# Kernel tuning notes

Hardware: AMD Instinct MI355X
Metric: run time of the kernel (lower is better)

Reference implementation:

```python
import jax, jax.numpy as jnp
import numpy as np

HEADS = 4
CH = 64  # hidden_channels (per-head out channels)
N_INT = 50000
N_LANE = 400000
E_PO = 400000
E_ADJ = 200000


def setup_inputs() -> dict:
    key = jax.random.key(0)
    ks = iter(jax.random.split(key, 32))
    rn = lambda shape, s=0.1: jax.random.normal(next(ks), shape, dtype=jnp.float32) * s
    inp = {
        'x_int': rn((N_INT, 16), 1.0),
        'x_lane': rn((N_LANE, 12), 1.0),
        'h0': jnp.zeros((N_INT, CH), jnp.float32),
        'enc_int_W': rn((16, CH)), 'enc_int_b': jnp.zeros((CH,), jnp.float32),
        'enc_lane_W': rn((12, CH)), 'enc_lane_b': jnp.zeros((CH,), jnp.float32),
        'Wsrc_po': rn((CH, HEADS * CH)), 'Wdst_po': rn((CH, HEADS * CH)),
        'att_src_po': rn((HEADS, CH)), 'att_dst_po': rn((HEADS, CH)),
        'bias_po': jnp.zeros((HEADS * CH,), jnp.float32),
        'Wsrc_adj': rn((CH, HEADS * CH)), 'Wdst_adj': rn((CH, HEADS * CH)),
        'att_src_adj': rn((HEADS, CH)), 'att_dst_adj': rn((HEADS, CH)),
        'bias_adj': jnp.zeros((HEADS * CH,), jnp.float32),
        'gru_W_ih': rn((3 * CH, HEADS * CH)), 'gru_W_hh': rn((3 * CH, CH)),
        'gru_b_ih': jnp.zeros((3 * CH,), jnp.float32), 'gru_b_hh': jnp.zeros((3 * CH,), jnp.float32),
        'W_pi': rn((CH, 8)), 'b_pi': jnp.zeros((8,), jnp.float32),
        'W_v': rn((CH, 1)), 'b_v': jnp.zeros((1,), jnp.float32),
        'src_po': jax.random.randint(next(ks), (E_PO,), 0, N_LANE),
        'dst_po': jax.random.randint(next(ks), (E_PO,), 0, N_INT),
        'src_adj': jax.random.randint(next(ks), (E_ADJ,), 0, N_INT),
        'dst_adj': jax.random.randint(next(ks), (E_ADJ,), 0, N_INT),
    }
    return inp


def gat_conv(x_src, x_dst, src, dst, Wsrc, Wdst, a_src, a_dst, bias, n_dst):
    # PyG GATConv (bipartite, concat=True, no self loops), negative_slope=0.2
    hs = (x_src @ Wsrc).reshape(-1, HEADS, CH)  # [Ns,H,C]
    hd = (x_dst @ Wdst).reshape(-1, HEADS, CH)  # [Nd,H,C]
    a_s = jnp.einsum('nhc,hc->nh', hs, a_src)   # [Ns,H]
    a_d = jnp.einsum('nhc,hc->nh', hd, a_dst)   # [Nd,H]
    alpha = jax.nn.leaky_relu(a_s[src] + a_d[dst], 0.2)        # [E,H]
    amax = jax.ops.segment_max(alpha, dst, num_segments=n_dst)  # [Nd,H]
    ex = jnp.exp(alpha - amax[dst])
    den = jax.ops.segment_sum(ex, dst, num_segments=n_dst)
    w = ex / den[dst]                                           # [E,H] softmax per dst
    msg = hs[src] * w[:, :, None]                               # [E,H,C]
    out = jax.ops.segment_sum(msg, dst, num_segments=n_dst)     # [Nd,H,C]
    return out.reshape(n_dst, HEADS * CH) + bias


def gru_cell(x, h, W_ih, W_hh, b_ih, b_hh):
    gi = x @ W_ih.T + b_ih
    gh = h @ W_hh.T + b_hh
    i_r, i_z, i_n = jnp.split(gi, 3, axis=1)
    h_r, h_z, h_n = jnp.split(gh, 3, axis=1)
    r = jax.nn.sigmoid(i_r + h_r)
    z = jax.nn.sigmoid(i_z + h_z)
    n = jnp.tanh(i_n + r * h_n)
    return (1.0 - z) * n + z * h


def reference(x_int, x_lane, h0, enc_int_W, enc_int_b, enc_lane_W, enc_lane_b,
              Wsrc_po, Wdst_po, att_src_po, att_dst_po, bias_po,
              Wsrc_adj, Wdst_adj, att_src_adj, att_dst_adj, bias_adj,
              gru_W_ih, gru_W_hh, gru_b_ih, gru_b_hh,
              W_pi, b_pi, W_v, b_v,
              src_po, dst_po, src_adj, dst_adj):
    # per-type encoders + ReLU
    e_int = jax.nn.relu(x_int @ enc_int_W + enc_int_b)    # [N_int,CH]
    e_lane = jax.nn.relu(x_lane @ enc_lane_W + enc_lane_b)  # [N_lane,CH]
    # HeteroConv aggr='sum' over relations targeting 'intersection'
    o_po = gat_conv(e_lane, e_int, src_po, dst_po, Wsrc_po, Wdst_po,
                    att_src_po, att_dst_po, bias_po, N_INT)
    o_adj = gat_conv(e_int, e_int, src_adj, dst_adj, Wsrc_adj, Wdst_adj,
                     att_src_adj, att_dst_adj, bias_adj, N_INT)
    inter = jax.nn.relu(o_po + o_adj)  # dropout = identity (deterministic eval)
    h_new = gru_cell(inter, h0, gru_W_ih, gru_W_hh, gru_b_ih, gru_b_hh)
    logits = h_new @ W_pi + b_pi
    value = h_new @ W_v + b_v
    return logits, value, h_new
```

## Files before the change

### kernel.cpp

```cpp
#include <hip/hip_runtime.h>

#define NI 50000
#define NL 400000
#define EPO 400000
#define EADJ 200000
#define NLB 1563
#define NIB 196

typedef unsigned int u32;
typedef unsigned short u16;
typedef short bf16x8 __attribute__((ext_vector_type(8)));
typedef float f32x4 __attribute__((ext_vector_type(4)));

__device__ __forceinline__ float bf2f(u16 h){ return __uint_as_float(((u32)h)<<16); }
__device__ __forceinline__ u16 f2bf(float f){
  u32 u = __float_as_uint(f);
  u += 0x7FFFu + ((u>>16)&1u);
  return (u16)(u>>16);
}
__device__ __forceinline__ u32 pack2(float a, float b){
  return (u32)f2bf(a) | ((u32)f2bf(b)<<16);
}

__device__ __forceinline__ float b2_val(
    const float* __restrict__ W_ih, const float* __restrict__ W_hh, int m, int k)
{
  if(k < 256){ return (m<192) ? W_ih[m*256+k] : 0.f; }
  int kk = k-256;
  if(m<128) return W_hh[m*64+kk];
  if(m>=192) return W_hh[(m-64)*64+kk];
  return 0.f;
}

__global__ __launch_bounds__(256) void k0_prep(
    const float* __restrict__ Wsrc_po, const float* __restrict__ att_src_po,
    const float* __restrict__ Wdst_po, const float* __restrict__ att_dst_po,
    const float* __restrict__ Wsrc_adj, const float* __restrict__ att_src_adj,
    const float* __restrict__ Wdst_adj, const float* __restrict__ att_dst_adj,
    const float* __restrict__ W_ih, const float* __restrict__ W_hh,
    const float* __restrict__ bias_po, const float* __restrict__ bias_adj,
    const float* __restrict__ b_ih, const float* __restrict__ b_hh,
    float* __restrict__ v4, u16* __restrict__ WheadT, u16* __restrict__ B2F,
    float* __restrict__ bias_comb, float* __restrict__ bias2,
    int* __restrict__ cnt)
{
  const int T0 = 1024, T1 = 4*64*128, T2 = 10*16*64*8;
  const int TC = 2*NI;
  int total = T0 + T1 + T2 + 256 + 256 + TC;
  for(int t = blockIdx.x*256 + threadIdx.x; t < total; t += gridDim.x*256){
    if(t < T0){
      int which = t>>8, hc = t&255, h = hc>>6, c = hc&63;
      const float *W, *att;
      if(which==0){ W=Wsrc_po;  att=att_src_po; }
      else if(which==1){ W=Wdst_po;  att=att_dst_po; }
      else if(which==2){ W=Wsrc_adj; att=att_src_adj; }
      else { W=Wdst_adj; att=att_dst_adj; }
      float s=0.f;
      for(int j=0;j<64;j++) s += W[c*256 + h*64 + j]*att[h*64+j];
      v4[which*256 + hc] = s;
    } else if(t < T0 + T1){
      int i = t - T0; int h = i>>13, rem = i&8191, m = rem>>7, k = rem&127;
      float val = (k<64) ? Wsrc_po[k*256 + h*64 + m]
                         : Wsrc_adj[(k-64)*256 + h*64 + m];
      WheadT[i] = f2bf(val);
    } else if(t < T0 + T1 + T2){
      int i = t - (T0+T1);
      int j = i&7;
      int u4 = i>>3;
      int kstep = u4>>10, rem = u4&1023, tile = rem>>6, lane = rem&63;
      int col = tile*16 + (lane&15);
      int k = kstep*32 + (lane>>4)*8 + j;
      B2F[i] = f2bf(b2_val(W_ih, W_hh, col, k));
    } else if(t < T0 + T1 + T2 + 256){
      int m = t - (T0+T1+T2);
      bias_comb[m] = bias_po[m] + bias_adj[m];
    } else if(t < T0 + T1 + T2 + 512){
      int m = t - (T0+T1+T2+256);
      float v;
      if(m<128) v = b_ih[m] + b_hh[m];
      else if(m<192) v = b_ih[m];
      else v = b_hh[m-64];
      bias2[m] = v;
    } else {
      cnt[t - (T0+T1+T2+512)] = 0;
    }
  }
}

__global__ __launch_bounds__(256) void k_enc(
    const float* __restrict__ x_lane, const float* __restrict__ Wl, const float* __restrict__ bl,
    const float* __restrict__ x_int,  const float* __restrict__ Wi, const float* __restrict__ bi,
    const float* __restrict__ v_sp, const float* __restrict__ v_dp,
    const float* __restrict__ v_sa, const float* __restrict__ v_da,
    u16* __restrict__ e_lane, float* __restrict__ a_s_po,
    u16* __restrict__ e_int, float* __restrict__ a_dp, float* __restrict__ a_sa,
    float* __restrict__ a_da)
{
  __shared__ uint4 st4[8][256];
  int t = threadIdx.x;
  int blk = blockIdx.x;
  if(blk < NLB){
    int row = blk*256 + t;
    float xv[12];
    if(row < NL){
      const float4* xp = (const float4*)(x_lane + (size_t)row*12);
      float4 x0 = xp[0], x1 = xp[1], x2 = xp[2];
      xv[0]=x0.x; xv[1]=x0.y; xv[2]=x0.z; xv[3]=x0.w;
      xv[4]=x1.x; xv[5]=x1.y; xv[6]=x1.z; xv[7]=x1.w;
      xv[8]=x2.x; xv[9]=x2.y; xv[10]=x2.z; xv[11]=x2.w;
    } else {
#pragma unroll
      for(int k=0;k<12;k++) xv[k]=0.f;
    }
    float as0=0.f, as1=0.f, as2=0.f, as3=0.f;
#pragma unroll
    for(int c8=0;c8<8;c8++){
      float acc[8];
#pragma unroll
      for(int j=0;j<8;j++) acc[j]=bl[c8*8+j];
#pragma unroll
      for(int k=0;k<12;k++){
        float xk = xv[k];
#pragma unroll
        for(int j=0;j<8;j++) acc[j] += xk*Wl[k*64 + c8*8 + j];
      }
      float e[8];
#pragma unroll
      for(int j=0;j<8;j++){
        e[j] = fmaxf(acc[j], 0.f);
        int c = c8*8+j;
        as0 += e[j]*v_sp[c];
        as1 += e[j]*v_sp[64+c];
        as2 += e[j]*v_sp[128+c];
        as3 += e[j]*v_sp[192+c];
      }
      uint4 P;
      P.x = pack2(e[0],e[1]); P.y = pack2(e[2],e[3]);
      P.z = pack2(e[4],e[5]); P.w = pack2(e[6],e[7]);
      st4[c8][t] = P;
    }
    if(row < NL){
      float4 A; A.x=as0; A.y=as1; A.z=as2; A.w=as3;
      *(float4*)(a_s_po + (size_t)row*4) = A;
    }
    __syncthreads();
    uint4* outp = (uint4*)e_lane + (size_t)blk*2048;
    int rowlim = NL - blk*256;
#pragma unroll
    for(int i=0;i<8;i++){
      int idx = i*256 + t;
      int r = idx>>3, g = idx&7;
      if(r < rowlim) outp[idx] = st4[g][r];
    }
  } else {
    int b2 = blk - NLB;
    int row = b2*256 + t;
    float xv[16];
    if(row < NI){
      const float4* xp = (const float4*)(x_int + (size_t)row*16);
#pragma unroll
      for(int q=0;q<4;q++){
        float4 xq = xp[q];
        xv[q*4]=xq.x; xv[q*4+1]=xq.y; xv[q*4+2]=xq.z; xv[q*4+3]=xq.w;
      }
    } else {
#pragma unroll
      for(int k=0;k<16;k++) xv[k]=0.f;
    }
    float ad0=0,ad1=0,ad2=0,ad3=0, sa0=0,sa1=0,sa2=0,sa3=0, da0=0,da1=0,da2=0,da3=0;
#pragma unroll
    for(int c8=0;c8<8;c8++){
      float acc[8];
#pragma unroll
      for(int j=0;j<8;j++) acc[j]=bi[c8*8+j];
#pragma unroll
      for(int k=0;k<16;k++){
        float xk = xv[k];
#pragma unroll
        for(int j=0;j<8;j++) acc[j] += xk*Wi[k*64 + c8*8 + j];
      }
      float e[8];
#pragma unroll
      for(int j=0;j<8;j++){
        e[j] = fmaxf(acc[j], 0.f);
        int c = c8*8+j;
        ad0 += e[j]*v_dp[c];   ad1 += e[j]*v_dp[64+c];  ad2 += e[j]*v_dp[128+c];  ad3 += e[j]*v_dp[192+c];
        sa0 += e[j]*v_sa[c];   sa1 += e[j]*v_sa[64+c];  sa2 += e[j]*v_sa[128+c];  sa3 += e[j]*v_sa[192+c];
        da0 += e[j]*v_da[c];   da1 += e[j]*v_da[64+c];  da2 += e[j]*v_da[128+c];  da3 += e[j]*v_da[192+c];
      }
      uint4 P;
      P.x = pack2(e[0],e[1]); P.y = pack2(e[2],e[3]);
      P.z = pack2(e[4],e[5]); P.w = pack2(e[6],e[7]);
      st4[c8][t] = P;
    }
    if(row < NI){
      float4 A;
      A.x=ad0; A.y=ad1; A.z=ad2; A.w=ad3; *(float4*)(a_dp + (size_t)row*4) = A;
      A.x=sa0; A.y=sa1; A.z=sa2; A.w=sa3; *(float4*)(a_sa + (size_t)row*4) = A;
      A.x=da0; A.y=da1; A.z=da2; A.w=da3; *(float4*)(a_da + (size_t)row*4) = A;
    }
    __syncthreads();
    uint4* outp = (uint4*)e_int + (size_t)b2*2048;
    int rowlim = NI - b2*256;
#pragma unroll
    for(int i=0;i<8;i++){
      int idx = i*256 + t;
      int r = idx>>3, g = idx&7;
      if(r < rowlim) outp[idx] = st4[g][r];
    }
  }
}

__global__ __launch_bounds__(256) void k3_hist(
    const int* __restrict__ dst_po, const int* __restrict__ dst_adj, int* __restrict__ cnt)
{
  int i = blockIdx.x*256 + threadIdx.x;
  if(i < EPO) atomicAdd(&cnt[dst_po[i]], 1);
  else if(i < EPO+EADJ) atomicAdd(&cnt[NI + dst_adj[i-EPO]], 1);
}

__global__ __launch_bounds__(1024) void k4a_scan(
    const int* __restrict__ cnt, int* __restrict__ offA, int* __restrict__ bsum)
{
  __shared__ int s[1024];
  int y = blockIdx.y;
  int i = blockIdx.x*1024 + threadIdx.x;
  int v = (i<NI) ? cnt[y*NI+i] : 0;
  s[threadIdx.x]=v;
  __syncthreads();
  for(int o=1;o<1024;o<<=1){
    int t = (threadIdx.x>=o) ? s[threadIdx.x-o] : 0;
    __syncthreads();
    s[threadIdx.x] += t;
    __syncthreads();
  }
  if(i<NI) offA[y*NI+i] = s[threadIdx.x]-v;
  if(threadIdx.x==1023) bsum[y*64+blockIdx.x] = s[1023];
}

__global__ __launch_bounds__(128) void k4b_scanb(int* __restrict__ bsum)
{
  int y = threadIdx.x>>6, lane = threadIdx.x&63;
  int v = (lane<49) ? bsum[y*64+lane] : 0;
  int orig = v;
#pragma unroll
  for(int o=1;o<64;o<<=1){
    int t = __shfl_up(v,o,64);
    if(lane>=o) v += t;
  }
  if(lane<49) bsum[y*64+lane] = v-orig;
}

__global__ __launch_bounds__(1024) void k4c_add(
    int* __restrict__ offA, int* __restrict__ cur, const int* __restrict__ bsum)
{
  int y = blockIdx.y;
  int i = blockIdx.x*1024 + threadIdx.x;
  if(i<NI){
    int o = offA[y*NI+i] + bsum[y*64+blockIdx.x];
    offA[y*NI+i]=o;
    cur[y*NI+i]=o;
  }
}

__global__ __launch_bounds__(256) void k5_scatter(
    const int* __restrict__ src_po, const int* __restrict__ dst_po,
    const int* __restrict__ src_adj, const int* __restrict__ dst_adj,
    const float* __restrict__ a_s_po, const float* __restrict__ a_d_po,
    const float* __restrict__ a_s_adj, const float* __restrict__ a_d_adj,
    int* __restrict__ cur, int* __restrict__ csr_po, int* __restrict__ csr_adj,
    float* __restrict__ pw_po, float* __restrict__ pw_adj)
{
  int i = blockIdx.x*256 + threadIdx.x;
  if(i < EPO){
    int s = src_po[i];
    int d = dst_po[i];
    int p = atomicAdd(&cur[d],1);
    csr_po[p] = s;
    float4 as = *(const float4*)(a_s_po + (size_t)s*4);
    float4 ad = *(const float4*)(a_d_po + (size_t)d*4);
    float4 pv;
    float x;
    x = as.x+ad.x; pv.x = __expf(x>0.f?x:0.2f*x);
    x = as.y+ad.y; pv.y = __expf(x>0.f?x:0.2f*x);
    x = as.z+ad.z; pv.z = __expf(x>0.f?x:0.2f*x);
    x = as.w+ad.w; pv.w = __expf(x>0.f?x:0.2f*x);
    *(float4*)(pw_po + (size_t)p*4) = pv;
  } else if(i < EPO+EADJ){
    int e = i-EPO;
    int s = src_adj[e];
    int d = dst_adj[e];
    int p = atomicAdd(&cur[NI+d],1);
    csr_adj[p] = s;
    float4 as = *(const float4*)(a_s_adj + (size_t)s*4);
    float4 ad = *(const float4*)(a_d_adj + (size_t)d*4);
    float4 pv;
    float x;
    x = as.x+ad.x; pv.x = __expf(x>0.f?x:0.2f*x);
    x = as.y+ad.y; pv.y = __expf(x>0.f?x:0.2f*x);
    x = as.z+ad.z; pv.z = __expf(x>0.f?x:0.2f*x);
    x = as.w+ad.w; pv.w = __expf(x>0.f?x:0.2f*x);
    *(float4*)(pw_adj + (size_t)p*4) = pv;
  }
}

__device__ __forceinline__ void agg_rel(
    int beg, int n, int lane,
    const int* __restrict__ csr, const float* __restrict__ pw,
    const u16* __restrict__ emat, u16* __restrict__ aggrow)
{
  float l0=0,l1=0,l2=0,l3=0;
  float c0=0,c1=0,c2=0,c3=0;
  for(int base=0;base<n;base+=64){
    int m = n-base; if(m>64) m=64;
    int sv_ = (lane<m) ? csr[beg+base+lane] : 0;
    int t2=0;
    for(; t2+1<m; t2+=2){
      int s0 = __shfl(sv_, t2, 64);
      int s1 = __shfl(sv_, t2+1, 64);
      float4 p0 = *(const float4*)(pw + (size_t)(beg+base+t2)*4);
      float4 p1 = *(const float4*)(pw + (size_t)(beg+base+t2+1)*4);
      float e0 = bf2f(emat[(size_t)s0*64+lane]);
      float e1 = bf2f(emat[(size_t)s1*64+lane]);
      c0 += p0.x*e0; c1 += p0.y*e0; c2 += p0.z*e0; c3 += p0.w*e0;
      l0 += p0.x;    l1 += p0.y;    l2 += p0.z;    l3 += p0.w;
      c0 += p1.x*e1; c1 += p1.y*e1; c2 += p1.z*e1; c3 += p1.w*e1;
      l0 += p1.x;    l1 += p1.y;    l2 += p1.z;    l3 += p1.w;
    }
    if(t2<m){
      int s0 = __shfl(sv_, t2, 64);
      float4 p0 = *(const float4*)(pw + (size_t)(beg+base+t2)*4);
      float e0 = bf2f(emat[(size_t)s0*64+lane]);
      c0 += p0.x*e0; c1 += p0.y*e0; c2 += p0.z*e0; c3 += p0.w*e0;
      l0 += p0.x;    l1 += p0.y;    l2 += p0.z;    l3 += p0.w;
    }
  }
  aggrow[lane]       = f2bf(n>0 ? c0/l0 : 0.f);
  aggrow[64+lane]    = f2bf(n>0 ? c1/l1 : 0.f);
  aggrow[128+lane]   = f2bf(n>0 ? c2/l2 : 0.f);
  aggrow[192+lane]   = f2bf(n>0 ? c3/l3 : 0.f);
}

__global__ __launch_bounds__(256) void k6_agg(
    const int* __restrict__ off, const int* __restrict__ cnt,
    const int* __restrict__ csr_po, const int* __restrict__ csr_adj,
    const float* __restrict__ pw_po, const float* __restrict__ pw_adj,
    const u16* __restrict__ e_lane, const u16* __restrict__ e_int,
    u16* __restrict__ agg)
{
  int wave=threadIdx.x>>6, lane=threadIdx.x&63;
  int d = blockIdx.x*4 + wave;
  if(d>=NI) return;
  agg_rel(off[d],    cnt[d],    lane, csr_po,  pw_po,  e_lane, agg + (size_t)d*512);
  agg_rel(off[NI+d], cnt[NI+d], lane, csr_adj, pw_adj, e_int,  agg + (size_t)d*512 + 256);
}

__global__ __launch_bounds__(256) void gemm_head(
    const u16* __restrict__ agg, const u16* __restrict__ WheadT,
    const float* __restrict__ bias, u16* __restrict__ inter256)
{
  __shared__ u16 As[64][136];
  __shared__ u16 Bs[64][136];
  int t=threadIdx.x, wave=t>>6, lane=t&63;
  int h = blockIdx.y;
  int row0 = blockIdx.x*64;
  int r = lane&15, q = lane>>4;
  const uint4* Bsrc = (const uint4*)(WheadT + (size_t)h*8192);
#pragma unroll
  for(int it=0; it<4; it++){
    int idx = it*256 + t;
    int brow = idx>>4, u4 = idx&15;
    *(uint4*)&Bs[brow][u4*8] = Bsrc[idx];
    int grow = row0 + brow;
    uint4 v = {0,0,0,0};
    if(grow < NI){
      int co = (u4<8) ? (h*64 + u4*8) : (256 + h*64 + (u4-8)*8);
      v = *(const uint4*)(agg + (size_t)grow*512 + co);
    }
    *(uint4*)&As[brow][u4*8] = v;
  }
  __syncthreads();
  f32x4 acc0={0,0,0,0}, acc1={0,0,0,0}, acc2={0,0,0,0}, acc3={0,0,0,0};
#pragma unroll
  for(int ks=0; ks<4; ks++){
    bf16x8 af = *(const bf16x8*)&As[wave*16 + r][q*8 + ks*32];
    bf16x8 b0 = *(const bf16x8*)&Bs[ 0 + r][q*8 + ks*32];
    bf16x8 b1 = *(const bf16x8*)&Bs[16 + r][q*8 + ks*32];
    bf16x8 b2 = *(const bf16x8*)&Bs[32 + r][q*8 + ks*32];
    bf16x8 b3 = *(const bf16x8*)&Bs[48 + r][q*8 + ks*32];
    acc0 = __builtin_amdgcn_mfma_f32_16x16x32_bf16(af,b0,acc0,0,0,0);
    acc1 = __builtin_amdgcn_mfma_f32_16x16x32_bf16(af,b1,acc1,0,0,0);
    acc2 = __builtin_amdgcn_mfma_f32_16x16x32_bf16(af,b2,acc2,0,0,0);
    acc3 = __builtin_amdgcn_mfma_f32_16x16x32_bf16(af,b3,acc3,0,0,0);
  }
  int crow_base = row0 + wave*16 + q*4;
#pragma unroll
  for(int t2=0;t2<4;t2++){
    f32x4 a = (t2==0)?acc0 : (t2==1)?acc1 : (t2==2)?acc2 : acc3;
    int col = h*64 + t2*16 + r;
    float bcol = bias[col];
#pragma unroll
    for(int rr=0;rr<4;rr++){
      int row = crow_base + rr;
      if(row < NI)
        inter256[(size_t)row*256 + col] = f2bf(fmaxf(a[rr]+bcol, 0.f));
    }
  }
}

__global__ __launch_bounds__(256) void k9_gru(
    const u16* __restrict__ inter256, const uint4* __restrict__ B2F,
    const float* __restrict__ bias2, const float* __restrict__ h0,
    const float* __restrict__ Wpi, const float* __restrict__ bpi,
    const float* __restrict__ Wv, const float* __restrict__ bvp,
    float* __restrict__ out)
{
  int t=threadIdx.x, w=t>>6, lane=t&63;
  int r = lane&15, q = lane>>4;
  int row0 = blockIdx.x*64;
  int arow = row0 + w*16 + r;
  int arc = arow < NI ? arow : NI-1;
  const u16* Aptr = inter256 + (size_t)arc*256 + q*8;
  const float* h0r = h0 + (size_t)arc*64 + q*8;
  f32x4 acc[16];
#pragma unroll
  for(int i=0;i<16;i++) acc[i] = (f32x4){0,0,0,0};
#pragma unroll
  for(int ks=0; ks<10; ks++){
    bf16x8 af;
    if(ks < 8){
      af = *(const bf16x8*)(Aptr + ks*32);
    } else {
      const float* hp = h0r + (ks-8)*32;
      float4 f0 = *(const float4*)(hp);
      float4 f1 = *(const float4*)(hp+4);
      uint4 P;
      P.x = pack2(f0.x,f0.y); P.y = pack2(f0.z,f0.w);
      P.z = pack2(f1.x,f1.y); P.w = pack2(f1.z,f1.w);
      *(uint4*)&af = P;
    }
    const uint4* bp = B2F + ks*1024 + lane;
#pragma unroll
    for(int tt=0;tt<16;tt++){
      uint4 bu = bp[tt*64];
      bf16x8 bf; *(uint4*)&bf = bu;
      acc[tt] = __builtin_amdgcn_mfma_f32_16x16x32_bf16(af, bf, acc[tt], 0,0,0);
    }
  }
  float pk[4][8];
  float pv[4];
#pragma unroll
  for(int rr=0;rr<4;rr++){
    pv[rr]=0.f;
#pragma unroll
    for(int j=0;j<8;j++) pk[rr][j]=0.f;
  }
  int rbase = row0 + w*16 + q*4;
#pragma unroll
  for(int t2=0;t2<4;t2++){
    int c = t2*16 + r;
    float b0 = bias2[c], b1 = bias2[64+c], b2 = bias2[128+c], b3 = bias2[192+c];
    float wp[8];
#pragma unroll
    for(int j=0;j<8;j++) wp[j] = Wpi[c*8+j];
    float wv = Wv[c];
#pragma unroll
    for(int rr=0;rr<4;rr++){
      int row = rbase + rr;
      float g0 = acc[t2][rr]    + b0;
      float g1 = acc[t2+4][rr]  + b1;
      float g2 = acc[t2+8][rr]  + b2;
      float g3 = acc[t2+12][rr] + b3;
      float h0v = (row < NI) ? h0[(size_t)row*64 + c] : 0.f;
      float rg = 1.f/(1.f+__expf(-g0));
      float zg = 1.f/(1.f+__expf(-g1));
      float e2 = __expf(2.f*(g2 + rg*g3));
      float ng = 1.f - 2.f/(e2+1.f);
      float h = (1.f-zg)*ng + zg*h0v;
      if(row < NI) out[450000 + (size_t)row*64 + c] = h;
#pragma unroll
      for(int j=0;j<8;j++) pk[rr][j] += h*wp[j];
      pv[rr] += h*wv;
    }
  }
#pragma unroll
  for(int o=1;o<16;o<<=1){
#pragma unroll
    for(int rr=0;rr<4;rr++){
#pragma unroll
      for(int j=0;j<8;j++) pk[rr][j] += __shfl_xor(pk[rr][j], o, 64);
      pv[rr] += __shfl_xor(pv[rr], o, 64);
    }
  }
  if(r==0){
#pragma unroll
    for(int rr=0;rr<4;rr++){
      int row = rbase + rr;
      if(row < NI){
#pragma unroll
        for(int j=0;j<8;j++) out[(size_t)row*8 + j] = pk[rr][j] + bpi[j];
        out[400000 + row] = pv[rr] + bvp[0];
      }
    }
  }
}

extern "C" void kernel_launch(void* const* d_in, const int* in_sizes, int n_in,
                              void* d_out, int out_size, void* d_ws, size_t ws_size,
                              hipStream_t stream) {
  const float* x_int      = (const float*)d_in[0];
  const float* x_lane     = (const float*)d_in[1];
  const float* h0         = (const float*)d_in[2];
  const float* enc_int_W  = (const float*)d_in[3];
  const float* enc_int_b  = (const float*)d_in[4];
  const float* enc_lane_W = (const float*)d_in[5];
  const float* enc_lane_b = (const float*)d_in[6];
  const float* Wsrc_po    = (const float*)d_in[7];
  const float* Wdst_po    = (const float*)d_in[8];
  const float* att_src_po = (const float*)d_in[9];
  const float* att_dst_po = (const float*)d_in[10];
  const float* bias_po    = (const float*)d_in[11];
  const float* Wsrc_adj   = (const float*)d_in[12];
  const float* Wdst_adj   = (const float*)d_in[13];
  const float* att_src_adj= (const float*)d_in[14];
  const float* att_dst_adj= (const float*)d_in[15];
  const float* bias_adj   = (const float*)d_in[16];
  const float* gru_W_ih   = (const float*)d_in[17];
  const float* gru_W_hh   = (const float*)d_in[18];
  const float* gru_b_ih   = (const float*)d_in[19];
  const float* gru_b_hh   = (const float*)d_in[20];
  const float* W_pi       = (const float*)d_in[21];
  const float* b_pi       = (const float*)d_in[22];
  const float* W_v        = (const float*)d_in[23];
  const float* b_v        = (const float*)d_in[24];
  const int* src_po  = (const int*)d_in[25];
  const int* dst_po  = (const int*)d_in[26];
  const int* src_adj = (const int*)d_in[27];
  const int* dst_adj = (const int*)d_in[28];
  float* out = (float*)d_out;

  char* w = (char*)d_ws;
  size_t ofs = 0;
  auto alloc = [&](size_t bytes)->char*{
    char* p = w + ofs;
    ofs = (ofs + bytes + 255) & ~(size_t)255;
    return p;
  };
  u16*  e_lane   = (u16*)alloc((size_t)NL*64*2);
  u16*  e_int    = (u16*)alloc((size_t)NI*64*2);
  float* a_s_po  = (float*)alloc((size_t)NL*4*4);
  float* a_d_po  = (float*)alloc((size_t)NI*4*4);
  float* a_s_adj = (float*)alloc((size_t)NI*4*4);
  float* a_d_adj = (float*)alloc((size_t)NI*4*4);
  int*  cnt      = (int*)alloc((size_t)2*NI*4);
  int*  offA     = (int*)alloc((size_t)2*NI*4);
  int*  cur      = (int*)alloc((size_t)2*NI*4);
  int*  csr_po   = (int*)alloc((size_t)EPO*4);
  int*  csr_adj  = (int*)alloc((size_t)EADJ*4);
  float* pw_po   = (float*)alloc((size_t)EPO*4*4);
  float* pw_adj  = (float*)alloc((size_t)EADJ*4*4);
  int*  bsum     = (int*)alloc(2*64*4);
  u16*  agg      = (u16*)alloc((size_t)NI*512*2);
  u16*  inter256 = (u16*)alloc((size_t)NI*256*2);
  u16*  WheadT   = (u16*)alloc(4*64*128*2);
  u16*  B2F      = (u16*)alloc(10*16*64*8*2);
  float* v4      = (float*)alloc(4*256*4);
  float* bias_comb = (float*)alloc(256*4);
  float* bias2   = (float*)alloc(256*4);
  (void)ws_size; (void)n_in; (void)in_sizes; (void)out_size;

  k0_prep<<<256, 256, 0, stream>>>(
      Wsrc_po, att_src_po, Wdst_po, att_dst_po,
      Wsrc_adj, att_src_adj, Wdst_adj, att_dst_adj,
      gru_W_ih, gru_W_hh, bias_po, bias_adj, gru_b_ih, gru_b_hh,
      v4, WheadT, B2F, bias_comb, bias2, cnt);
  k_enc<<<NLB+NIB, 256, 0, stream>>>(
      x_lane, enc_lane_W, enc_lane_b,
      x_int, enc_int_W, enc_int_b,
      v4 + 0, v4 + 256, v4 + 512, v4 + 768,
      e_lane, a_s_po, e_int, a_d_po, a_s_adj, a_d_adj);
  k3_hist<<<(EPO+EADJ+255)/256, 256, 0, stream>>>(dst_po, dst_adj, cnt);
  k4a_scan<<<dim3(49,2), 1024, 0, stream>>>(cnt, offA, bsum);
  k4b_scanb<<<1, 128, 0, stream>>>(bsum);
  k4c_add<<<dim3(49,2), 1024, 0, stream>>>(offA, cur, bsum);
  k5_scatter<<<(EPO+EADJ+255)/256, 256, 0, stream>>>(src_po, dst_po, src_adj, dst_adj,
      a_s_po, a_d_po, a_s_adj, a_d_adj,
      cur, csr_po, csr_adj, pw_po, pw_adj);
  k6_agg<<<(NI+3)/4, 256, 0, stream>>>(offA, cnt, csr_po, csr_adj,
      pw_po, pw_adj, e_lane, e_int, agg);
  gemm_head<<<dim3((NI+63)/64, 4), 256, 0, stream>>>(agg, WheadT, bias_comb, inter256);
  k9_gru<<<(NI+63)/64, 256, 0, stream>>>(inter256, (const uint4*)B2F, bias2, h0,
      W_pi, b_pi, W_v, b_v, out);
}
```

Baseline: 379.9 us.

## Split encoder into lane/int kernels with 8 threads per row and shuffle reductions

Replaces the fused encoder kernel (one thread per row computing all 64 channels, then staging through LDS) with two kernels. In each, 8 threads share a row and each computes 8 channels. The attention dot products are reduced with xor shuffles, and results are stored directly without shared memory or a barrier. The lane kernel keeps its weights in registers, processes 16 rows per thread group, and prefetches the next row's input. This trades more threads per row and shuffle overhead for less per-thread work, lower LDS use and better load balance, at the cost of an extra kernel launch.

After: 393.3 us. 3.5% more time.

```diff
diff --git a/kernel.cpp b/kernel.cpp
--- a/kernel.cpp
+++ b/kernel.cpp
@@ -4,8 +4,6 @@
 #define NL 400000
 #define EPO 400000
 #define EADJ 200000
-#define NLB 1563
-#define NIB 196
 
 typedef unsigned int u32;
 typedef unsigned short u16;
@@ -87,77 +85,111 @@
   }
 }
 
-__global__ __launch_bounds__(256) void k_enc(
-    const float* __restrict__ x_lane, const float* __restrict__ Wl, const float* __restrict__ bl,
-    const float* __restrict__ x_int,  const float* __restrict__ Wi, const float* __restrict__ bi,
-    const float* __restrict__ v_sp, const float* __restrict__ v_dp,
-    const float* __restrict__ v_sa, const float* __restrict__ v_da,
-    u16* __restrict__ e_lane, float* __restrict__ a_s_po,
-    u16* __restrict__ e_int, float* __restrict__ a_dp, float* __restrict__ a_sa,
-    float* __restrict__ a_da)
-{
-  __shared__ uint4 st4[8][256];
+#define K1_ITER 16
+__global__ __launch_bounds__(256) void k1_enc(
+    const float* __restrict__ x, const float* __restrict__ W, const float* __restrict__ b,
+    const float* __restrict__ v_sp, u16* __restrict__ e_out, float* __restrict__ a_s)
+{
   int t = threadIdx.x;
-  int blk = blockIdx.x;
-  if(blk < NLB){
-    int row = blk*256 + t;
+  int wv = t>>6, l = t&63;
+  int g = l&7, m = l>>3;
+  float wreg[12][8], breg[8];
+#pragma unroll
+  for(int k=0;k<12;k++){
+    float4 w0 = *(const float4*)(W + k*64 + g*8);
+    float4 w1 = *(const float4*)(W + k*64 + g*8 + 4);
+    wreg[k][0]=w0.x; wreg[k][1]=w0.y; wreg[k][2]=w0.z; wreg[k][3]=w0.w;
+    wreg[k][4]=w1.x; wreg[k][5]=w1.y; wreg[k][6]=w1.z; wreg[k][7]=w1.w;
+  }
+  {
+    float4 b0 = *(const float4*)(b + g*8);
+    float4 b1 = *(const float4*)(b + g*8 + 4);
+    breg[0]=b0.x; breg[1]=b0.y; breg[2]=b0.z; breg[3]=b0.w;
+    breg[4]=b1.x; breg[5]=b1.y; breg[6]=b1.z; breg[7]=b1.w;
+  }
+  int rowbase = blockIdx.x*(4*8*K1_ITER) + wv*(8*K1_ITER) + m;
+  int row = rowbase;
+  float4 xa={0,0,0,0}, xb={0,0,0,0}, xc={0,0,0,0};
+  if(row < NL){
+    const float4* xp = (const float4*)(x + (size_t)row*12);
+    xa = xp[0]; xb = xp[1]; xc = xp[2];
+  }
+#pragma unroll
+  for(int it=0; it<K1_ITER; it++){
+    int nrow = row + 8;
+    float4 na={0,0,0,0}, nb={0,0,0,0}, nc={0,0,0,0};
+    if(it+1 < K1_ITER && nrow < NL){
+      const float4* xp = (const float4*)(x + (size_t)nrow*12);
+      na = xp[0]; nb = xp[1]; nc = xp[2];
+    }
     float xv[12];
+    xv[0]=xa.x; xv[1]=xa.y; xv[2]=xa.z; xv[3]=xa.w;
+    xv[4]=xb.x; xv[5]=xb.y; xv[6]=xb.z; xv[7]=xb.w;
+    xv[8]=xc.x; xv[9]=xc.y; xv[10]=xc.z; xv[11]=xc.w;
+    float acc[8];
+#pragma unroll
+    for(int j=0;j<8;j++) acc[j]=breg[j];
+#pragma unroll
+    for(int k=0;k<12;k++){
+      float xk = xv[k];
+#pragma unroll
+      for(int j=0;j<8;j++) acc[j] += xk*wreg[k][j];
+    }
+    float e[8];
+#pragma unroll
+    for(int j=0;j<8;j++) e[j] = fmaxf(acc[j], 0.f);
+    float as[4];
+#pragma unroll
+    for(int h=0;h<4;h++){
+      float4 v0 = *(const float4*)(v_sp + h*64 + g*8);
+      float4 v1 = *(const float4*)(v_sp + h*64 + g*8 + 4);
+      as[h] = e[0]*v0.x + e[1]*v0.y + e[2]*v0.z + e[3]*v0.w
+            + e[4]*v1.x + e[5]*v1.y + e[6]*v1.z + e[7]*v1.w;
+    }
+#pragma unroll
+    for(int o=1;o<8;o<<=1){
+#pragma unroll
+      for(int h=0;h<4;h++) as[h] += __shfl_xor(as[h], o, 64);
+    }
     if(row < NL){
-      const float4* xp = (const float4*)(x_lane + (size_t)row*12);
-      float4 x0 = xp[0], x1 = xp[1], x2 = xp[2];
-      xv[0]=x0.x; xv[1]=x0.y; xv[2]=x0.z; xv[3]=x0.w;
-      xv[4]=x1.x; xv[5]=x1.y; xv[6]=x1.z; xv[7]=x1.w;
-      xv[8]=x2.x; xv[9]=x2.y; xv[10]=x2.z; xv[11]=x2.w;
-    } else {
-#pragma unroll
-      for(int k=0;k<12;k++) xv[k]=0.f;
-    }
-    float as0=0.f, as1=0.f, as2=0.f, as3=0.f;
-#pragma unroll
-    for(int c8=0;c8<8;c8++){
-      float acc[8];
-#pragma unroll
-      for(int j=0;j<8;j++) acc[j]=bl[c8*8+j];
-#pragma unroll
-      for(int k=0;k<12;k++){
-        float xk = xv[k];
-#pragma unroll
-        for(int j=0;j<8;j++) acc[j] += xk*Wl[k*64 + c8*8 + j];
-      }
-      float e[8];
-#pragma unroll
-      for(int j=0;j<8;j++){
-        e[j] = fmaxf(acc[j], 0.f);
-        int c = c8*8+j;
-        as0 += e[j]*v_sp[c];
-        as1 += e[j]*v_sp[64+c];
-        as2 += e[j]*v_sp[128+c];
-        as3 += e[j]*v_sp[192+c];
-      }
       uint4 P;
       P.x = pack2(e[0],e[1]); P.y = pack2(e[2],e[3]);
       P.z = pack2(e[4],e[5]); P.w = pack2(e[6],e[7]);
-      st4[c8][t] = P;
-    }
-    if(row < NL){
-      float4 A; A.x=as0; A.y=as1; A.z=as2; A.w=as3;
-      *(float4*)(a_s_po + (size_t)row*4) = A;
-    }
-    __syncthreads();
-    uint4* outp = (uint4*)e_lane + (size_t)blk*2048;
-    int rowlim = NL - blk*256;
-#pragma unroll
-    for(int i=0;i<8;i++){
-      int idx = i*256 + t;
-      int r = idx>>3, g = idx&7;
-      if(r < rowlim) outp[idx] = st4[g][r];
-    }
-  } else {
-    int b2 = blk - NLB;
-    int row = b2*256 + t;
+      ((uint4*)e_out)[(size_t)row*8 + g] = P;
+      if(g==0){
+        float4 A; A.x=as[0]; A.y=as[1]; A.z=as[2]; A.w=as[3];
+        *(float4*)(a_s + (size_t)row*4) = A;
+      }
+    }
+    xa=na; xb=nb; xc=nc;
+    row = nrow;
+  }
+}
+
+#define K2_ITER 4
+__global__ __launch_bounds__(256) void k2_enc(
+    const float* __restrict__ x, const float* __restrict__ W, const float* __restrict__ b,
+    const float* __restrict__ v_dp, const float* __restrict__ v_sa, const float* __restrict__ v_da,
+    u16* __restrict__ e_out, float* __restrict__ a_dp, float* __restrict__ a_sa,
+    float* __restrict__ a_da)
+{
+  int t = threadIdx.x;
+  int wv = t>>6, l = t&63;
+  int g = l&7, m = l>>3;
+  float breg[8];
+  {
+    float4 b0 = *(const float4*)(b + g*8);
+    float4 b1 = *(const float4*)(b + g*8 + 4);
+    breg[0]=b0.x; breg[1]=b0.y; breg[2]=b0.z; breg[3]=b0.w;
+    breg[4]=b1.x; breg[5]=b1.y; breg[6]=b1.z; breg[7]=b1.w;
+  }
+  int rowbase = blockIdx.x*(4*8*K2_ITER) + wv*(8*K2_ITER) + m;
+#pragma unroll
+  for(int it=0; it<K2_ITER; it++){
+    int row = rowbase + it*8;
     float xv[16];
     if(row < NI){
-      const float4* xp = (const float4*)(x_int + (size_t)row*16);
+      const float4* xp = (const float4*)(x + (size_t)row*16);
 #pragma unroll
       for(int q=0;q<4;q++){
         float4 xq = xp[q];
@@ -167,46 +199,54 @@
 #pragma unroll
       for(int k=0;k<16;k++) xv[k]=0.f;
     }
-    float ad0=0,ad1=0,ad2=0,ad3=0, sa0=0,sa1=0,sa2=0,sa3=0, da0=0,da1=0,da2=0,da3=0;
-#pragma unroll
-    for(int c8=0;c8<8;c8++){
-      float acc[8];
-#pragma unroll
-      for(int j=0;j<8;j++) acc[j]=bi[c8*8+j];
-#pragma unroll
-      for(int k=0;k<16;k++){
-        float xk = xv[k];
-#pragma unroll
-        for(int j=0;j<8;j++) acc[j] += xk*Wi[k*64 + c8*8 + j];
+    float acc[8];
+#pragma unroll
+    for(int j=0;j<8;j++) acc[j]=breg[j];
+#pragma unroll
+    for(int k=0;k<16;k++){
+      float4 w0 = *(const float4*)(W + k*64 + g*8);
+      float4 w1 = *(const float4*)(W + k*64 + g*8 + 4);
+      float xk = xv[k];
+      acc[0] += xk*w0.x; acc[1] += xk*w0.y; acc[2] += xk*w0.z; acc[3] += xk*w0.w;
+      acc[4] += xk*w1.x; acc[5] += xk*w1.y; acc[6] += xk*w1.z; acc[7] += xk*w1.w;
+    }
+    float e[8];
+#pragma unroll
+    for(int j=0;j<8;j++) e[j] = fmaxf(acc[j], 0.f);
+    float ad[4], sa[4], da[4];
+#pragma unroll
+    for(int h=0;h<4;h++){
+      float4 v0, v1;
+      v0 = *(const float4*)(v_dp + h*64 + g*8); v1 = *(const float4*)(v_dp + h*64 + g*8 + 4);
+      ad[h] = e[0]*v0.x + e[1]*v0.y + e[2]*v0.z + e[3]*v0.w
+            + e[4]*v1.x + e[5]*v1.y + e[6]*v1.z + e[7]*v1.w;
+      v0 = *(const float4*)(v_sa + h*64 + g*8); v1 = *(const float4*)(v_sa + h*64 + g*8 + 4);
+      sa[h] = e[0]*v0.x + e[1]*v0.y + e[2]*v0.z + e[3]*v0.w
+            + e[4]*v1.x + e[5]*v1.y + e[6]*v1.z + e[7]*v1.w;
+      v0 = *(const float4*)(v_da + h*64 + g*8); v1 = *(const float4*)(v_da + h*64 + g*8 + 4);
+      da[h] = e[0]*v0.x + e[1]*v0.y + e[2]*v0.z + e[3]*v0.w
+            + e[4]*v1.x + e[5]*v1.y + e[6]*v1.z + e[7]*v1.w;
+    }
+#pragma unroll
+    for(int o=1;o<8;o<<=1){
+#pragma unroll
+      for(int h=0;h<4;h++){
+        ad[h] += __shfl_xor(ad[h], o, 64);
+        sa[h] += __shfl_xor(sa[h], o, 64);
+        da[h] += __shfl_xor(da[h], o, 64);
       }
-      float e[8];
-#pragma unroll
-      for(int j=0;j<8;j++){
-        e[j] = fmaxf(acc[j], 0.f);
-        int c = c8*8+j;
-        ad0 += e[j]*v_dp[c];   ad1 += e[j]*v_dp[64+c];  ad2 += e[j]*v_dp[128+c];  ad3 += e[j]*v_dp[192+c];
-        sa0 += e[j]*v_sa[c];   sa1 += e[j]*v_sa[64+c];  sa2 += e[j]*v_sa[128+c];  sa3 += e[j]*v_sa[192+c];
-        da0 += e[j]*v_da[c];   da1 += e[j]*v_da[64+c];  da2 += e[j]*v_da[128+c];  da3 += e[j]*v_da[192+c];
-      }
+    }
+    if(row < NI){
       uint4 P;
       P.x = pack2(e[0],e[1]); P.y = pack2(e[2],e[3]);
       P.z = pack2(e[4],e[5]); P.w = pack2(e[6],e[7]);
-      st4[c8][t] = P;
-    }
-    if(row < NI){
-      float4 A;
-      A.x=ad0; A.y=ad1; A.z=ad2; A.w=ad3; *(float4*)(a_dp + (size_t)row*4) = A;
-      A.x=sa0; A.y=sa1; A.z=sa2; A.w=sa3; *(float4*)(a_sa + (size_t)row*4) = A;
-      A.x=da0; A.y=da1; A.z=da2; A.w=da3; *(float4*)(a_da + (size_t)row*4) = A;
-    }
-    __syncthreads();
-    uint4* outp = (uint4*)e_int + (size_t)b2*2048;
-    int rowlim = NI - b2*256;
-#pragma unroll
-    for(int i=0;i<8;i++){
-      int idx = i*256 + t;
-      int r = idx>>3, g = idx&7;
-      if(r < rowlim) outp[idx] = st4[g][r];
+      ((uint4*)e_out)[(size_t)row*8 + g] = P;
+      if(g==0){
+        float4 A;
+        A.x=ad[0]; A.y=ad[1]; A.z=ad[2]; A.w=ad[3]; *(float4*)(a_dp + (size_t)row*4) = A;
+        A.x=sa[0]; A.y=sa[1]; A.z=sa[2]; A.w=sa[3]; *(float4*)(a_sa + (size_t)row*4) = A;
+        A.x=da[0]; A.y=da[1]; A.z=da[2]; A.w=da[3]; *(float4*)(a_da + (size_t)row*4) = A;
+      }
     }
   }
 }
@@ -574,11 +614,11 @@
       Wsrc_adj, att_src_adj, Wdst_adj, att_dst_adj,
       gru_W_ih, gru_W_hh, bias_po, bias_adj, gru_b_ih, gru_b_hh,
       v4, WheadT, B2F, bias_comb, bias2, cnt);
-  k_enc<<<NLB+NIB, 256, 0, stream>>>(
-      x_lane, enc_lane_W, enc_lane_b,
-      x_int, enc_int_W, enc_int_b,
-      v4 + 0, v4 + 256, v4 + 512, v4 + 768,
-      e_lane, a_s_po, e_int, a_d_po, a_s_adj, a_d_adj);
+  k1_enc<<<(NL + 511)/512, 256, 0, stream>>>(x_lane, enc_lane_W, enc_lane_b,
+      v4 + 0, e_lane, a_s_po);
+  k2_enc<<<(NI + 127)/128, 256, 0, stream>>>(x_int, enc_int_W, enc_int_b,
+      v4 + 256, v4 + 512, v4 + 768,
+      e_int, a_d_po, a_s_adj, a_d_adj);
   k3_hist<<<(EPO+EADJ+255)/256, 256, 0, stream>>>(dst_po, dst_adj, cnt);
   k4a_scan<<<dim3(49,2), 1024, 0, stream>>>(cnt, offA, bsum);
   k4b_scanb<<<1, 128, 0, stream>>>(bsum);
```
